# Kernel tuning notes

Hardware: AMD Instinct MI355X
Metric: run time of the kernel (lower is better)

Reference implementation:

```python
import jax, jax.numpy as jnp
import numpy as np

L = 2048
D_MODEL = 1024
D_INNER = 1024
DT_RANK = 64
D_STATE = 16


def setup_inputs() -> dict:
    key = jax.random.key(0)
    ks = jax.random.split(key, 5)
    proj_dim = DT_RANK + 2 * D_INNER * D_STATE
    x = jax.random.normal(ks[0], (L, D_INNER), dtype=jnp.float32)
    # equinox Linear weights are [out, in]
    W_in = jax.random.normal(ks[1], (proj_dim, D_MODEL), dtype=jnp.float32) / np.sqrt(D_MODEL)
    W_delta = jax.random.normal(ks[2], (D_INNER, DT_RANK), dtype=jnp.float32) / np.sqrt(DT_RANK)
    W_out = jax.random.normal(ks[3], (D_MODEL, D_INNER), dtype=jnp.float32) / np.sqrt(D_INNER)
    # A_log initialized as log(1..d_state) tiled over d_inner, as in __init__
    A_log = jnp.log(jnp.tile(jnp.arange(1, D_STATE + 1, dtype=jnp.float32), (D_INNER, 1)))
    D = jnp.ones((D_INNER,), dtype=jnp.float32)
    return {"x": x, "W_in": W_in, "W_delta": W_delta, "A_log": A_log, "D": D, "W_out": W_out}


def reference(x, W_in, W_delta, A_log, D, W_out):
    Lq, d_inner = x.shape
    d_state = A_log.shape[1]
    dt_rank = W_delta.shape[1]

    A = -jnp.exp(A_log.astype(jnp.float32))          # [d_inner, d_state]
    Df = D.astype(jnp.float32)                        # [d_inner]

    dbc = x @ W_in.T                                  # [L, dt_rank + 2*d_inner*d_state]
    delta_lr = dbc[:, :dt_rank]
    B = dbc[:, dt_rank:dt_rank + d_inner * d_state].reshape(Lq, d_inner, d_state)
    C = dbc[:, dt_rank + d_inner * d_state:].reshape(Lq, d_inner, d_state)
    delta = jax.nn.softplus(delta_lr @ W_delta.T)     # [L, d_inner]

    # discretize (ZOH for A, Euler for B*u), as in standard Mamba selective_scan
    deltaA = jnp.exp(delta[:, :, None] * A)           # [L, d_inner, d_state]
    deltaBu = delta[:, :, None] * B * x[:, :, None]   # [L, d_inner, d_state]

    def step(h, inp):
        dA, dBu, c = inp
        h = dA * h + dBu                               # [d_inner, d_state]
        y = jnp.sum(h * c, axis=-1)                    # [d_inner]
        return h, y

    h0 = jnp.zeros((d_inner, d_state), dtype=deltaA.dtype)
    _, ys = jax.lax.scan(step, h0, (deltaA, deltaBu, C))  # ys: [L, d_inner]

    y = ys + x * Df
    return y @ W_out.T                                 # [L, d_model]
```

## Files before the change

kernel.cpp:

```cpp
#include <hip/hip_runtime.h>
#include <cstdint>
#include <cstddef>

#define L_SEQ 2048
#define DI 1024
#define DM 1024
#define RK 64
#define DS 16
#define NBC 32768
#define NCHUNK 128
#define TCHUNK 16

using f32x4  = __attribute__((ext_vector_type(4))) float;
using bf16x8 = __attribute__((ext_vector_type(8))) short;

typedef const __attribute__((address_space(1))) void gas_void;
typedef __attribute__((address_space(3))) void las_void;

#define GLL16(gp, lp) __builtin_amdgcn_global_load_lds( \
    (gas_void*)(uintptr_t)(gp), (las_void*)(uintptr_t)(lp), 16, 0, 0)

__device__ __forceinline__ unsigned short f2bf(float f) {
  unsigned u = __builtin_bit_cast(unsigned, f);
  u += 0x7fffu + ((u >> 16) & 1u);
  return (unsigned short)(u >> 16);
}
__device__ __forceinline__ float bflo(unsigned u) { return __builtin_bit_cast(float, u << 16); }
__device__ __forceinline__ float bfhi(unsigned u) { return __builtin_bit_cast(float, u & 0xffff0000u); }
__device__ __forceinline__ float softplusf(float z) {
  return (z > 20.f) ? z : log1pf(expf(z));
}

__global__ void cast_bf16_kernel(const float* __restrict__ in,
                                 unsigned short* __restrict__ out, int n8) {
  int i = blockIdx.x * blockDim.x + threadIdx.x;
  if (i >= n8) return;
  const f32x4* p = (const f32x4*)(in + (size_t)i * 8);
  f32x4 a = p[0], b = p[1];
  union { unsigned short us[8]; uint4 v; } r;
#pragma unroll
  for (int j = 0; j < 4; ++j) r.us[j] = f2bf(a[j]);
#pragma unroll
  for (int j = 0; j < 4; ++j) r.us[4 + j] = f2bf(b[j]);
  *(uint4*)(out + (size_t)i * 8) = r.v;
}

template <bool OUT_BF16>
__global__ __launch_bounds__(256) void gemm_bt(
    const unsigned short* __restrict__ A,
    const unsigned short* __restrict__ Bm,
    void* __restrict__ Cv, int K, int ldc) {
  __shared__ unsigned short As[128 * 32];
  __shared__ unsigned short Bs[128 * 32];
  const int tid = threadIdx.x;
  const int lane = tid & 63;
  const int wave = tid >> 6;
  const int wm = (wave >> 1) * 64, wn = (wave & 1) * 64;
  const int m0 = blockIdx.y * 128, n0 = blockIdx.x * 128;
  const int lr = lane & 15, lk = (lane >> 4) * 8;

  const int srow = tid >> 2;
  const int scol = (tid & 3) * 8;
  const unsigned short* gA = A + (size_t)(m0 + srow) * K + scol;
  const unsigned short* gB = Bm + (size_t)(n0 + srow) * K + scol;
  unsigned short* lA0 = &As[tid * 8];
  unsigned short* lA1 = &As[2048 + tid * 8];
  unsigned short* lB0 = &Bs[tid * 8];
  unsigned short* lB1 = &Bs[2048 + tid * 8];

  f32x4 acc[4][4];
#pragma unroll
  for (int m = 0; m < 4; ++m)
#pragma unroll
    for (int n = 0; n < 4; ++n) acc[m][n] = f32x4{0.f, 0.f, 0.f, 0.f};

  for (int k0 = 0; k0 < K; k0 += 32) {
    GLL16(gA + k0, lA0);
    GLL16(gA + (size_t)64 * K + k0, lA1);
    GLL16(gB + k0, lB0);
    GLL16(gB + (size_t)64 * K + k0, lB1);
    __syncthreads();
    bf16x8 af[4], bfr[4];
#pragma unroll
    for (int m = 0; m < 4; ++m)
      af[m] = *(const bf16x8*)&As[(wm + m * 16 + lr) * 32 + lk];
#pragma unroll
    for (int n = 0; n < 4; ++n)
      bfr[n] = *(const bf16x8*)&Bs[(wn + n * 16 + lr) * 32 + lk];
#pragma unroll
    for (int m = 0; m < 4; ++m)
#pragma unroll
      for (int n = 0; n < 4; ++n)
        acc[m][n] = __builtin_amdgcn_mfma_f32_16x16x32_bf16(af[m], bfr[n], acc[m][n], 0, 0, 0);
    __syncthreads();
  }

  const int crow = (lane >> 4) * 4;
  const int ccol = lane & 15;
#pragma unroll
  for (int m = 0; m < 4; ++m)
#pragma unroll
    for (int n = 0; n < 4; ++n)
#pragma unroll
      for (int r = 0; r < 4; ++r) {
        int row = m0 + wm + m * 16 + crow + r;
        int col = n0 + wn + n * 16 + ccol;
        float v = acc[m][n][r];
        if (OUT_BF16)
          ((unsigned short*)Cv)[(size_t)row * ldc + col] = f2bf(v);
        else
          ((float*)Cv)[(size_t)row * ldc + col] = v;
      }
}

__global__ __launch_bounds__(256) void delta_lr_kernel(
    const float* __restrict__ x, const float* __restrict__ Win,
    float* __restrict__ dlr) {
  __shared__ float xs[16][65];
  __shared__ float ws[64][65];
  const int tid = threadIdx.x;
  const int t0 = blockIdx.x * 16;
  const int r = tid & 63, tg = tid >> 6;
  float a0 = 0.f, a1 = 0.f, a2 = 0.f, a3 = 0.f;
  for (int k0 = 0; k0 < DM; k0 += 64) {
    {
      int row = tid >> 4, col = (tid & 15) * 4;
      f32x4 v = *(const f32x4*)&x[(size_t)(t0 + row) * DM + k0 + col];
      xs[row][col] = v.x; xs[row][col + 1] = v.y; xs[row][col + 2] = v.z; xs[row][col + 3] = v.w;
    }
#pragma unroll
    for (int p = 0; p < 4; ++p) {
      int idx = tid + p * 256;
      int row = idx >> 4, col = (idx & 15) * 4;
      f32x4 v = *(const f32x4*)&Win[(size_t)row * DM + k0 + col];
      ws[row][col] = v.x; ws[row][col + 1] = v.y; ws[row][col + 2] = v.z; ws[row][col + 3] = v.w;
    }
    __syncthreads();
#pragma unroll 16
    for (int kk = 0; kk < 64; ++kk) {
      float wv = ws[r][kk];
      a0 += xs[tg * 4 + 0][kk] * wv;
      a1 += xs[tg * 4 + 1][kk] * wv;
      a2 += xs[tg * 4 + 2][kk] * wv;
      a3 += xs[tg * 4 + 3][kk] * wv;
    }
    __syncthreads();
  }
  dlr[(size_t)(t0 + tg * 4 + 0) * RK + r] = a0;
  dlr[(size_t)(t0 + tg * 4 + 1) * RK + r] = a1;
  dlr[(size_t)(t0 + tg * 4 + 2) * RK + r] = a2;
  dlr[(size_t)(t0 + tg * 4 + 3) * RK + r] = a3;
}

__global__ __launch_bounds__(256) void delta_kernel(
    const float* __restrict__ dlr, const float* __restrict__ Wd,
    float* __restrict__ delta) {
  __shared__ float dl[16][65];
  __shared__ float wd[64][65];
  const int tid = threadIdx.x;
  const int i0 = blockIdx.x * 64;
  const int t0 = blockIdx.y * 16;
  const int il = tid & 63, tg = tid >> 6;
  {
    int row = tid >> 4, col = (tid & 15) * 4;
    f32x4 v = *(const f32x4*)&dlr[(size_t)(t0 + row) * RK + col];
    dl[row][col] = v.x; dl[row][col + 1] = v.y; dl[row][col + 2] = v.z; dl[row][col + 3] = v.w;
  }
#pragma unroll
  for (int p = 0; p < 4; ++p) {
    int idx = tid + p * 256;
    int row = idx >> 4, col = (idx & 15) * 4;
    f32x4 v = *(const f32x4*)&Wd[(size_t)(i0 + row) * RK + col];
    wd[row][col] = v.x; wd[row][col + 1] = v.y; wd[row][col + 2] = v.z; wd[row][col + 3] = v.w;
  }
  __syncthreads();
  float a0 = 0.f, a1 = 0.f, a2 = 0.f, a3 = 0.f;
#pragma unroll 16
  for (int kk = 0; kk < 64; ++kk) {
    float wv = wd[il][kk];
    a0 += dl[tg * 4 + 0][kk] * wv;
    a1 += dl[tg * 4 + 1][kk] * wv;
    a2 += dl[tg * 4 + 2][kk] * wv;
    a3 += dl[tg * 4 + 3][kk] * wv;
  }
  delta[(size_t)(t0 + tg * 4 + 0) * DI + i0 + il] = softplusf(a0);
  delta[(size_t)(t0 + tg * 4 + 1) * DI + i0 + il] = softplusf(a1);
  delta[(size_t)(t0 + tg * 4 + 2) * DI + i0 + il] = softplusf(a2);
  delta[(size_t)(t0 + tg * 4 + 3) * DI + i0 + il] = softplusf(a3);
}

__global__ __launch_bounds__(256) void scan_pass1(
    const float* __restrict__ delta, const float* __restrict__ x,
    const unsigned short* __restrict__ dbc, const float* __restrict__ A_log,
    float* __restrict__ h_end, float* __restrict__ P_end) {
  const int c = blockIdx.x >> 2;
  const int d = ((blockIdx.x & 3) << 8) + threadIdx.x;
  float Av[16];
#pragma unroll
  for (int q = 0; q < 4; ++q) {
    f32x4 v = *(const f32x4*)&A_log[(size_t)d * 16 + q * 4];
    Av[q * 4 + 0] = -expf(v.x); Av[q * 4 + 1] = -expf(v.y);
    Av[q * 4 + 2] = -expf(v.z); Av[q * 4 + 3] = -expf(v.w);
  }
  float h[16], P[16];
#pragma unroll
  for (int s = 0; s < 16; ++s) { h[s] = 0.f; P[s] = 1.f; }
  const int t0 = c * TCHUNK, t1 = t0 + TCHUNK;
  uint4 b0 = *(const uint4*)&dbc[(size_t)t0 * NBC + d * 16];
  uint4 b1 = *(const uint4*)&dbc[(size_t)t0 * NBC + d * 16 + 8];
  float dlt = delta[(size_t)t0 * DI + d];
  float xv = x[(size_t)t0 * DI + d];
  for (int t = t0; t < t1; ++t) {
    int tn = (t + 1 < t1) ? t + 1 : t;
    uint4 nb0 = *(const uint4*)&dbc[(size_t)tn * NBC + d * 16];
    uint4 nb1 = *(const uint4*)&dbc[(size_t)tn * NBC + d * 16 + 8];
    float ndlt = delta[(size_t)tn * DI + d];
    float nxv = x[(size_t)tn * DI + d];
    float du = dlt * xv;
    unsigned bu[8] = {b0.x, b0.y, b0.z, b0.w, b1.x, b1.y, b1.z, b1.w};
#pragma unroll
    for (int s = 0; s < 16; ++s) {
      float dA = __expf(dlt * Av[s]);
      float Bv = (s & 1) ? bfhi(bu[s >> 1]) : bflo(bu[s >> 1]);
      h[s] = dA * h[s] + du * Bv;
      P[s] *= dA;
    }
    b0 = nb0; b1 = nb1; dlt = ndlt; xv = nxv;
  }
  float* he = &h_end[((size_t)c * DI + d) * 16];
  float* pe = &P_end[((size_t)c * DI + d) * 16];
#pragma unroll
  for (int q = 0; q < 4; ++q) {
    f32x4 vh = {h[q * 4 + 0], h[q * 4 + 1], h[q * 4 + 2], h[q * 4 + 3]};
    f32x4 vp = {P[q * 4 + 0], P[q * 4 + 1], P[q * 4 + 2], P[q * 4 + 3]};
    *(f32x4*)&he[q * 4] = vh;
    *(f32x4*)&pe[q * 4] = vp;
  }
}

__global__ void scan_pass2(const float* __restrict__ h_end,
                           const float* __restrict__ P_end,
                           float* __restrict__ h_in) {
  const int j = blockIdx.x * 256 + threadIdx.x;
  const int NS = DI * DS;
  float h = 0.f;
  for (int c = 0; c < NCHUNK; c += 4) {
    float P0 = P_end[(size_t)(c + 0) * NS + j], H0 = h_end[(size_t)(c + 0) * NS + j];
    float P1 = P_end[(size_t)(c + 1) * NS + j], H1 = h_end[(size_t)(c + 1) * NS + j];
    float P2 = P_end[(size_t)(c + 2) * NS + j], H2 = h_end[(size_t)(c + 2) * NS + j];
    float P3 = P_end[(size_t)(c + 3) * NS + j], H3 = h_end[(size_t)(c + 3) * NS + j];
    h_in[(size_t)(c + 0) * NS + j] = h; h = P0 * h + H0;
    h_in[(size_t)(c + 1) * NS + j] = h; h = P1 * h + H1;
    h_in[(size_t)(c + 2) * NS + j] = h; h = P2 * h + H2;
    h_in[(size_t)(c + 3) * NS + j] = h; h = P3 * h + H3;
  }
}

__global__ __launch_bounds__(256) void scan_pass3(
    const float* __restrict__ delta, const float* __restrict__ x,
    const unsigned short* __restrict__ dbc, const float* __restrict__ A_log,
    const float* __restrict__ Dvec, const float* __restrict__ h_in,
    unsigned short* __restrict__ ybf) {
  const int c = blockIdx.x >> 2;
  const int d = ((blockIdx.x & 3) << 8) + threadIdx.x;
  float Av[16];
#pragma unroll
  for (int q = 0; q < 4; ++q) {
    f32x4 v = *(const f32x4*)&A_log[(size_t)d * 16 + q * 4];
    Av[q * 4 + 0] = -expf(v.x); Av[q * 4 + 1] = -expf(v.y);
    Av[q * 4 + 2] = -expf(v.z); Av[q * 4 + 3] = -expf(v.w);
  }
  const float Df = Dvec[d];
  float h[16];
  const float* hi = &h_in[((size_t)c * DI + d) * 16];
#pragma unroll
  for (int q = 0; q < 4; ++q) {
    f32x4 v = *(const f32x4*)&hi[q * 4];
    h[q * 4 + 0] = v.x; h[q * 4 + 1] = v.y; h[q * 4 + 2] = v.z; h[q * 4 + 3] = v.w;
  }
  const int t0 = c * TCHUNK, t1 = t0 + TCHUNK;
  uint4 b0 = *(const uint4*)&dbc[(size_t)t0 * NBC + d * 16];
  uint4 b1 = *(const uint4*)&dbc[(size_t)t0 * NBC + d * 16 + 8];
  uint4 c0 = *(const uint4*)&dbc[(size_t)t0 * NBC + DI * DS + d * 16];
  uint4 c1 = *(const uint4*)&dbc[(size_t)t0 * NBC + DI * DS + d * 16 + 8];
  float dlt = delta[(size_t)t0 * DI + d];
  float xv = x[(size_t)t0 * DI + d];
  for (int t = t0; t < t1; ++t) {
    int tn = (t + 1 < t1) ? t + 1 : t;
    uint4 nb0 = *(const uint4*)&dbc[(size_t)tn * NBC + d * 16];
    uint4 nb1 = *(const uint4*)&dbc[(size_t)tn * NBC + d * 16 + 8];
    uint4 nc0 = *(const uint4*)&dbc[(size_t)tn * NBC + DI * DS + d * 16];
    uint4 nc1 = *(const uint4*)&dbc[(size_t)tn * NBC + DI * DS + d * 16 + 8];
    float ndlt = delta[(size_t)tn * DI + d];
    float nxv = x[(size_t)tn * DI + d];
    float du = dlt * xv;
    unsigned bu[8] = {b0.x, b0.y, b0.z, b0.w, b1.x, b1.y, b1.z, b1.w};
    unsigned cu[8] = {c0.x, c0.y, c0.z, c0.w, c1.x, c1.y, c1.z, c1.w};
    float yacc = 0.f;
#pragma unroll
    for (int s = 0; s < 16; ++s) {
      float dA = __expf(dlt * Av[s]);
      float Bv = (s & 1) ? bfhi(bu[s >> 1]) : bflo(bu[s >> 1]);
      float Cv = (s & 1) ? bfhi(cu[s >> 1]) : bflo(cu[s >> 1]);
      h[s] = dA * h[s] + du * Bv;
      yacc += h[s] * Cv;
    }
    ybf[(size_t)t * DI + d] = f2bf(yacc + xv * Df);
    b0 = nb0; b1 = nb1; c0 = nc0; c1 = nc1; dlt = ndlt; xv = nxv;
  }
}

extern "C" void kernel_launch(void* const* d_in, const int* in_sizes, int n_in,
                              void* d_out, int out_size, void* d_ws, size_t ws_size,
                              hipStream_t stream) {
  const float* x    = (const float*)d_in[0];
  const float* Win  = (const float*)d_in[1];
  const float* Wd   = (const float*)d_in[2];
  const float* Alog = (const float*)d_in[3];
  const float* Dv   = (const float*)d_in[4];
  const float* Wout = (const float*)d_in[5];
  float* out = (float*)d_out;

  char* ws = (char*)d_ws;
  size_t off = 0;
  auto walloc = [&](size_t bytes) -> void* {
    void* p = ws + off;
    off += (bytes + 255) & ~(size_t)255;
    return p;
  };
  unsigned short* x_bf    = (unsigned short*)walloc((size_t)L_SEQ * DI * 2);
  unsigned short* Wbc_bf  = (unsigned short*)walloc((size_t)NBC * DM * 2);
  unsigned short* Wout_bf = (unsigned short*)walloc((size_t)DM * DI * 2);
  unsigned short* dbc     = (unsigned short*)walloc((size_t)L_SEQ * NBC * 2);
  float* dlr   = (float*)walloc((size_t)L_SEQ * RK * 4);
  float* delta = (float*)walloc((size_t)L_SEQ * DI * 4);
  unsigned short* y_bf = (unsigned short*)walloc((size_t)L_SEQ * DI * 2);
  float* h_end = (float*)walloc((size_t)NCHUNK * DI * DS * 4);
  float* P_end = (float*)walloc((size_t)NCHUNK * DI * DS * 4);
  float* h_in  = (float*)walloc((size_t)NCHUNK * DI * DS * 4);

  cast_bf16_kernel<<<(L_SEQ * DI / 8 + 255) / 256, 256, 0, stream>>>(x, x_bf, L_SEQ * DI / 8);
  cast_bf16_kernel<<<((size_t)NBC * DM / 8 + 255) / 256, 256, 0, stream>>>(
      Win + (size_t)RK * DM, Wbc_bf, NBC * DM / 8);
  cast_bf16_kernel<<<(DM * DI / 8 + 255) / 256, 256, 0, stream>>>(Wout, Wout_bf, DM * DI / 8);

  delta_lr_kernel<<<L_SEQ / 16, 256, 0, stream>>>(x, Win, dlr);
  delta_kernel<<<dim3(DI / 64, L_SEQ / 16), 256, 0, stream>>>(dlr, Wd, delta);

  gemm_bt<true><<<dim3(NBC / 128, L_SEQ / 128), 256, 0, stream>>>(x_bf, Wbc_bf, dbc, DM, NBC);

  scan_pass1<<<NCHUNK * 4, 256, 0, stream>>>(delta, x, dbc, Alog, h_end, P_end);
  scan_pass2<<<DI * DS / 256, 256, 0, stream>>>(h_end, P_end, h_in);
  scan_pass3<<<NCHUNK * 4, 256, 0, stream>>>(delta, x, dbc, Alog, Dv, h_in, y_bf);

  gemm_bt<false><<<dim3(DI / 128, L_SEQ / 128), 256, 0, stream>>>(y_bf, Wout_bf, out, DM, DI);
}
```

Measured before the change: 540.8 us.

## Replace large B/C projection GEMM with 256x256-tile 4-stage pipelined MFMA kernel

```diff
diff --git a/kernel.cpp b/kernel.cpp
--- a/kernel.cpp
+++ b/kernel.cpp
@@ -20,6 +20,8 @@
 #define GLL16(gp, lp) __builtin_amdgcn_global_load_lds( \
     (gas_void*)(uintptr_t)(gp), (las_void*)(uintptr_t)(lp), 16, 0, 0)
 
+#define VMCNT(n) asm volatile("s_waitcnt vmcnt(" #n ")" ::: "memory")
+
 __device__ __forceinline__ unsigned short f2bf(float f) {
   unsigned u = __builtin_bit_cast(unsigned, f);
   u += 0x7fffu + ((u >> 16) & 1u);
@@ -43,6 +45,108 @@
 #pragma unroll
   for (int j = 0; j < 4; ++j) r.us[4 + j] = f2bf(b[j]);
   *(uint4*)(out + (size_t)i * 8) = r.v;
+}
+
+__global__ __launch_bounds__(512, 2) void gemm_big(
+    const unsigned short* __restrict__ A,
+    const unsigned short* __restrict__ Bm,
+    unsigned short* __restrict__ C) {
+  constexpr int K = 1024;
+  constexpr int KT = 32;
+  constexpr int LDC = NBC;
+  constexpr int GRID_N = 128;
+  __shared__ unsigned short lds[65536];
+
+  const int tid = threadIdx.x;
+  const int lane = tid & 63;
+  const int wave = tid >> 6;
+  const int wm = (wave >> 2) * 128;
+  const int wn = (wave & 3) * 64;
+  const int lr = lane & 15;
+  const int lkx = ((lane >> 4) ^ (lr & 3)) << 4;
+
+  const int b = blockIdx.x;
+  const int per = gridDim.x >> 3;
+  const int sw = (b & 7) * per + (b >> 3);
+  const int m0 = (sw / GRID_N) * 256;
+  const int n0 = (sw % GRID_N) * 256;
+
+  const int r0 = tid >> 2;
+  const int colsw = 8 * ((tid & 3) ^ (r0 & 3));
+  const unsigned short* gA0 = A + (size_t)(m0 + r0) * K + colsw;
+  const unsigned short* gA1 = gA0 + (size_t)128 * K;
+  const unsigned short* gB0 = Bm + (size_t)(n0 + r0) * K + colsw;
+  const unsigned short* gB1 = gB0 + (size_t)128 * K;
+
+  f32x4 acc[8][4];
+#pragma unroll
+  for (int m = 0; m < 8; ++m)
+#pragma unroll
+    for (int n = 0; n < 4; ++n) acc[m][n] = f32x4{0.f, 0.f, 0.f, 0.f};
+
+  auto stage = [&](int buf, int kt) {
+    const int kofs = kt * 32;
+    unsigned short* d = &lds[buf * 16384 + tid * 8];
+    GLL16(gA0 + kofs, d);
+    GLL16(gA1 + kofs, d + 4096);
+    GLL16(gB0 + kofs, d + 8192);
+    GLL16(gB1 + kofs, d + 12288);
+  };
+
+  auto compute = [&](int buf) {
+    const char* base = (const char*)lds + (size_t)buf * 32768;
+    bf16x8 af[8], bv[4];
+#pragma unroll
+    for (int m = 0; m < 8; ++m)
+      af[m] = *(const bf16x8*)(base + (wm + m * 16 + lr) * 64 + lkx);
+#pragma unroll
+    for (int n = 0; n < 4; ++n)
+      bv[n] = *(const bf16x8*)(base + 16384 + (wn + n * 16 + lr) * 64 + lkx);
+    __builtin_amdgcn_s_setprio(1);
+#pragma unroll
+    for (int m = 0; m < 8; ++m)
+#pragma unroll
+      for (int n = 0; n < 4; ++n)
+        acc[m][n] = __builtin_amdgcn_mfma_f32_16x16x32_bf16(af[m], bv[n], acc[m][n], 0, 0, 0);
+    __builtin_amdgcn_s_setprio(0);
+  };
+
+  stage(0, 0);
+  stage(1, 1);
+  stage(2, 2);
+  VMCNT(8);
+  __builtin_amdgcn_s_barrier();
+  __builtin_amdgcn_sched_barrier(0);
+
+#pragma unroll 4
+  for (int t = 0; t < KT - 3; ++t) {
+    stage((t + 3) & 3, t + 3);
+    compute(t & 3);
+    VMCNT(8);
+    __builtin_amdgcn_s_barrier();
+    __builtin_amdgcn_sched_barrier(0);
+  }
+  compute((KT - 3) & 3);
+  VMCNT(4);
+  __builtin_amdgcn_s_barrier();
+  __builtin_amdgcn_sched_barrier(0);
+  compute((KT - 2) & 3);
+  VMCNT(0);
+  __builtin_amdgcn_s_barrier();
+  __builtin_amdgcn_sched_barrier(0);
+  compute((KT - 1) & 3);
+
+  const int crow = (lane >> 4) * 4;
+#pragma unroll
+  for (int m = 0; m < 8; ++m)
+#pragma unroll
+    for (int n = 0; n < 4; ++n)
+#pragma unroll
+      for (int r = 0; r < 4; ++r) {
+        int row = m0 + wm + m * 16 + crow + r;
+        int col = n0 + wn + n * 16 + lr;
+        C[(size_t)row * LDC + col] = f2bf(acc[m][n][r]);
+      }
 }
 
 template <bool OUT_BF16>
@@ -347,7 +451,7 @@
   delta_lr_kernel<<<L_SEQ / 16, 256, 0, stream>>>(x, Win, dlr);
   delta_kernel<<<dim3(DI / 64, L_SEQ / 16), 256, 0, stream>>>(dlr, Wd, delta);
 
-  gemm_bt<true><<<dim3(NBC / 128, L_SEQ / 128), 256, 0, stream>>>(x_bf, Wbc_bf, dbc, DM, NBC);
+  gemm_big<<<(L_SEQ / 256) * (NBC / 256), 512, 0, stream>>>(x_bf, Wbc_bf, dbc);
 
   scan_pass1<<<NCHUNK * 4, 256, 0, stream>>>(delta, x, dbc, Alog, h_end, P_end);
   scan_pass2<<<DI * DS / 256, 256, 0, stream>>>(h_end, P_end, h_in);
```

New measurement: 506.3 us. 1.07x faster.
